# Kernel tuning notes

Hardware: AMD Instinct MI355X
Metric: run time of the kernel (lower is better)

## Reference

```python
import jax, jax.numpy as jnp
import numpy as np

N, E, F_IN, F_E, H, T = 100000, 1600000, 128, 16, 64, 32
NEG_SLOPE = 0.2


def setup_inputs() -> dict:
    key = jax.random.key(0)
    ks = jax.random.split(key, 24)
    s = 0.1
    inp = {
        'x': jax.random.normal(ks[0], (N, F_IN), jnp.float32),
        'edge_index': jax.random.randint(ks[1], (2, E), 0, N, dtype=jnp.int32),
        'edge_attr': jax.random.normal(ks[2], (E, F_E), jnp.float32),
        # GATConv layer 1 (heads=1)
        'W1': jax.random.normal(ks[3], (F_IN, H), jnp.float32) * s,
        'as1': jax.random.normal(ks[4], (H,), jnp.float32) * s,
        'ad1': jax.random.normal(ks[5], (H,), jnp.float32) * s,
        'We1': jax.random.normal(ks[6], (F_E, H), jnp.float32) * s,
        'ae1': jax.random.normal(ks[7], (H,), jnp.float32) * s,
        'b1': jnp.zeros((H,), jnp.float32),
        # GATConv layer 2
        'W2': jax.random.normal(ks[8], (H, H), jnp.float32) * s,
        'as2': jax.random.normal(ks[9], (H,), jnp.float32) * s,
        'ad2': jax.random.normal(ks[10], (H,), jnp.float32) * s,
        'We2': jax.random.normal(ks[11], (F_E, H), jnp.float32) * s,
        'ae2': jax.random.normal(ks[12], (H,), jnp.float32) * s,
        'b2': jnp.zeros((H,), jnp.float32),
        # classifier MLP (dropout in eval mode -> identity)
        'Wc1': jax.random.normal(ks[13], (H, H // 2), jnp.float32) * s,
        'bc1': jnp.zeros((H // 2,), jnp.float32),
        'Wc2': jax.random.normal(ks[14], (H // 2, T), jnp.float32) * s,
        'bc2': jnp.zeros((T,), jnp.float32),
    }
    return inp


def gat_conv(x, src, dst, edge_attr, W, a_s, a_d, We, a_e, b):
    """Single-head PyG-style GATConv with edge features and self-loops
    (self-loop edge_attr = mean of incoming edge_attr, fill_value='mean')."""
    n = x.shape[0]
    # self loops with mean incoming edge features
    deg = jax.ops.segment_sum(jnp.ones_like(dst, jnp.float32), dst, n)
    loop_attr = jax.ops.segment_sum(edge_attr, dst, n) / jnp.maximum(deg, 1.0)[:, None]
    loops = jnp.arange(n, dtype=src.dtype)
    src_f = jnp.concatenate([src, loops])
    dst_f = jnp.concatenate([dst, loops])
    ea = jnp.concatenate([edge_attr, loop_attr], axis=0)  # [E+N, F_E]
    h = x @ W                                             # [N, H]
    # attention logits per edge: alpha_src[j] + alpha_dst[i] + alpha_edge
    alpha = (h @ a_s)[src_f] + (h @ a_d)[dst_f] + (ea @ We) @ a_e
    alpha = jax.nn.leaky_relu(alpha, NEG_SLOPE)
    # segment softmax over incoming edges per destination node
    m = jax.ops.segment_max(alpha, dst_f, n)
    p = jnp.exp(alpha - m[dst_f])
    z = jax.ops.segment_sum(p, dst_f, n)
    w = p / z[dst_f]                                      # [E+N]
    out = jax.ops.segment_sum(w[:, None] * h[src_f], dst_f, n)
    return out + b


def reference(x, edge_index, edge_attr, W1, as1, ad1, We1, ae1, b1,
              W2, as2, ad2, We2, ae2, b2, Wc1, bc1, Wc2, bc2):
    src, dst = edge_index[0], edge_index[1]
    h = jax.nn.relu(gat_conv(x, src, dst, edge_attr, W1, as1, ad1, We1, ae1, b1))
    h = jax.nn.relu(gat_conv(h, src, dst, edge_attr, W2, as2, ad2, We2, ae2, b2))
    h = jax.nn.relu(h @ Wc1 + bc1)
    logits = h @ Wc2 + bc2
    return logits
```

## Files before the change

### kernel.cpp

```cpp
#include <hip/hip_runtime.h>
#include <hip/hip_bf16.h>
#include <hip/hip_fp16.h>

#define NEG_SLOPE 0.2f

__device__ __forceinline__ float leaky(float a) { return a > 0.f ? a : NEG_SLOPE * a; }

__global__ void compute_wvec(const float* __restrict__ We1, const float* __restrict__ ae1,
                             const float* __restrict__ We2, const float* __restrict__ ae2,
                             float* __restrict__ wv) {
    int t = threadIdx.x;
    if (t < 16) {
        float s = 0.f;
        for (int k = 0; k < 64; ++k) s += We1[t * 64 + k] * ae1[k];
        wv[t] = s;
    } else if (t < 32) {
        int f = t - 16;
        float s = 0.f;
        for (int k = 0; k < 64; ++k) s += We2[f * 64 + k] * ae2[k];
        wv[16 + f] = s;
    }
}

__global__ void pack_edges(const int* __restrict__ dst, const float* __restrict__ eattr,
                           const float* __restrict__ wv, int* __restrict__ deg,
                           uint2* __restrict__ meta, int E) {
    __shared__ float w1s[16], w2s[16];
    if (threadIdx.x < 16) w1s[threadIdx.x] = wv[threadIdx.x];
    else if (threadIdx.x < 32) w2s[threadIdx.x - 16] = wv[threadIdx.x];
    __syncthreads();
    int e = blockIdx.x * blockDim.x + threadIdx.x;
    if (e >= E) return;
    const float4* ep = (const float4*)(eattr + (size_t)e * 16);
    float4 q0 = ep[0], q1 = ep[1], q2 = ep[2], q3 = ep[3];
    float a[16] = {q0.x, q0.y, q0.z, q0.w, q1.x, q1.y, q1.z, q1.w,
                   q2.x, q2.y, q2.z, q2.w, q3.x, q3.y, q3.z, q3.w};
    float s1 = 0.f, s2 = 0.f;
#pragma unroll
    for (int f = 0; f < 16; ++f) { s1 += a[f] * w1s[f]; s2 += a[f] * w2s[f]; }
    unsigned int p1 = (unsigned int)__half_as_ushort(__float2half_rn(s1));
    unsigned int p2 = (unsigned int)__half_as_ushort(__float2half_rn(s2));
    int rank = atomicAdd(&deg[dst[e]], 1);
    meta[e] = make_uint2(p1 | (p2 << 16), (unsigned int)rank);
}

__global__ void scan_blocks(const int* __restrict__ deg, int* __restrict__ rowptr,
                            int* __restrict__ bsum, int n) {
    __shared__ int sh[1024];
    int i = blockIdx.x * 1024 + threadIdx.x;
    sh[threadIdx.x] = (i < n) ? deg[i] : 0;
    __syncthreads();
    for (int off = 1; off < 1024; off <<= 1) {
        int t = (threadIdx.x >= off) ? sh[threadIdx.x - off] : 0;
        __syncthreads();
        sh[threadIdx.x] += t;
        __syncthreads();
    }
    if (i < n) rowptr[i + 1] = sh[threadIdx.x];
    if (threadIdx.x == 1023) bsum[blockIdx.x] = sh[1023];
}

__global__ void scan_sums(int* __restrict__ bsum, int nb) {
    __shared__ int sh[1024];
    int t = threadIdx.x;
    int v = (t < nb) ? bsum[t] : 0;
    sh[t] = v;
    __syncthreads();
    for (int off = 1; off < 1024; off <<= 1) {
        int u = (t >= off) ? sh[t - off] : 0;
        __syncthreads();
        sh[t] += u;
        __syncthreads();
    }
    if (t < nb) bsum[t] = sh[t] - v;
}

__global__ void scan_finalize(int* __restrict__ rowptr, const int* __restrict__ bsum, int n) {
    int i = blockIdx.x * blockDim.x + threadIdx.x;
    if (i < n) rowptr[i + 1] += bsum[i >> 10];
    if (i == 0) rowptr[0] = 0;
}

__global__ __launch_bounds__(256) void route_edges(
    const int* __restrict__ src, const int* __restrict__ dst,
    const uint2* __restrict__ meta, const int* __restrict__ rowptr,
    uint2* __restrict__ recs, int E, int slice_sz) {
    int xcd = blockIdx.x & 7;
    int team = blockIdx.x >> 3;
    int teams = gridDim.x >> 3;
    int lo = xcd * slice_sz, hi = lo + slice_sz;
    for (int e = team * 256 + threadIdx.x; e < E; e += teams * 256) {
        int d = dst[e];
        if (d < lo || d >= hi) continue;
        uint2 m = meta[e];
        int pos = rowptr[d] + (int)m.y;
        recs[pos] = make_uint2((unsigned int)src[e], m.x);
    }
}

template <int K>
__global__ __launch_bounds__(256) void gemm_node(const float* __restrict__ X,
                                                 const float* __restrict__ W,
                                                 const float* __restrict__ a_s,
                                                 const float* __restrict__ a_d,
                                                 __half* __restrict__ Hout16,
                                                 float* __restrict__ ash,
                                                 float* __restrict__ adh, int n) {
    constexpr int KC = 64;
    __shared__ float xs[128 * 65];
    __shared__ float ws[KC * 64];
    int tid = threadIdx.x;
    int base = blockIdx.x * 128;
    int ct = tid & 7;
    int rt = tid >> 3;

    float acc[4][8];
#pragma unroll
    for (int i = 0; i < 4; ++i)
#pragma unroll
        for (int j = 0; j < 8; ++j) acc[i][j] = 0.f;

    for (int kc = 0; kc < K; kc += KC) {
#pragma unroll
        for (int p = 0; p < 8; ++p) {
            int idx = p * 256 + tid;
            int row = idx >> 4;
            int f4 = idx & 15;
            float4 q = make_float4(0.f, 0.f, 0.f, 0.f);
            if (base + row < n) q = *(const float4*)(X + (size_t)(base + row) * K + kc + f4 * 4);
            float* dp = xs + row * 65 + f4 * 4;
            dp[0] = q.x; dp[1] = q.y; dp[2] = q.z; dp[3] = q.w;
        }
#pragma unroll
        for (int p = 0; p < 4; ++p) {
            int idx = p * 256 + tid;
            int f = idx >> 4;
            int c4 = idx & 15;
            *(float4*)(ws + f * 64 + c4 * 4) =
                *(const float4*)(W + (size_t)(kc + f) * 64 + c4 * 4);
        }
        __syncthreads();
#pragma unroll 4
        for (int f = 0; f < KC; ++f) {
            float4 w0 = *(const float4*)(ws + f * 64 + ct * 8);
            float4 w1 = *(const float4*)(ws + f * 64 + ct * 8 + 4);
            float b0[8] = {w0.x, w0.y, w0.z, w0.w, w1.x, w1.y, w1.z, w1.w};
#pragma unroll
            for (int i = 0; i < 4; ++i) {
                float a = xs[(rt * 4 + i) * 65 + f];
#pragma unroll
                for (int j = 0; j < 8; ++j) acc[i][j] = fmaf(a, b0[j], acc[i][j]);
            }
        }
        __syncthreads();
    }

    float as_r[8], ad_r[8];
#pragma unroll
    for (int j = 0; j < 8; ++j) { as_r[j] = a_s[ct * 8 + j]; ad_r[j] = a_d[ct * 8 + j]; }
#pragma unroll
    for (int i = 0; i < 4; ++i) {
        int r = base + rt * 4 + i;
        float ps = 0.f, pd = 0.f;
#pragma unroll
        for (int j = 0; j < 8; ++j) {
            ps = fmaf(acc[i][j], as_r[j], ps);
            pd = fmaf(acc[i][j], ad_r[j], pd);
        }
        ps += __shfl_xor(ps, 1); pd += __shfl_xor(pd, 1);
        ps += __shfl_xor(ps, 2); pd += __shfl_xor(pd, 2);
        ps += __shfl_xor(ps, 4); pd += __shfl_xor(pd, 4);
        if (r < n) {
            union { __half h[8]; uint4 u; } pk;
#pragma unroll
            for (int j = 0; j < 8; ++j) pk.h[j] = __float2half_rn(acc[i][j]);
            *(uint4*)(Hout16 + (size_t)r * 64 + ct * 8) = pk.u;
            if (ct == 0) { ash[r] = ps; adh[r] = pd; }
        }
    }
}

template <int LAYER>
__global__ __launch_bounds__(256) void gat_aggregate(
    const __half* __restrict__ Hf, const float* __restrict__ ash, const float* __restrict__ adh,
    const int* __restrict__ rowptr, const uint2* __restrict__ recs,
    const float* __restrict__ bias, float* __restrict__ outp, int n) {
    int wave = threadIdx.x >> 6;
    int lane = threadIdx.x & 63;
    int i = blockIdx.x * 4 + wave;
    if (i >= n) return;
    int start = rowptr[i], end = rowptr[i + 1];
    float adi = adh[i];

    float acc = 0.f;
    float zl = 0.f, seal = 0.f;

    for (int c = start; c < end; c += 64) {
        int cnt = min(64, end - c);
        int s_l = 0;
        float p_l = 0.f;
        if (lane < cnt) {
            uint2 r = recs[c + lane];
            s_l = (int)r.x;
            unsigned short u = (LAYER == 0) ? (unsigned short)(r.y & 0xffffu)
                                            : (unsigned short)(r.y >> 16);
            float e = __half2float(__ushort_as_half(u));
            float p = __expf(leaky(ash[s_l] + adi + e));
            p_l = p;
            zl += p;
            seal += e;
        }
        int k = 0;
        for (; k + 4 <= cnt; k += 4) {
            int s0 = __builtin_amdgcn_readlane(s_l, k);
            int s1 = __builtin_amdgcn_readlane(s_l, k + 1);
            int s2 = __builtin_amdgcn_readlane(s_l, k + 2);
            int s3 = __builtin_amdgcn_readlane(s_l, k + 3);
            float p0 = __uint_as_float(__builtin_amdgcn_readlane((int)__float_as_uint(p_l), k));
            float p1 = __uint_as_float(__builtin_amdgcn_readlane((int)__float_as_uint(p_l), k + 1));
            float p2 = __uint_as_float(__builtin_amdgcn_readlane((int)__float_as_uint(p_l), k + 2));
            float p3 = __uint_as_float(__builtin_amdgcn_readlane((int)__float_as_uint(p_l), k + 3));
            float v0 = __half2float(Hf[(size_t)s0 * 64 + lane]);
            float v1 = __half2float(Hf[(size_t)s1 * 64 + lane]);
            float v2 = __half2float(Hf[(size_t)s2 * 64 + lane]);
            float v3 = __half2float(Hf[(size_t)s3 * 64 + lane]);
            acc = fmaf(p0, v0, acc);
            acc = fmaf(p1, v1, acc);
            acc = fmaf(p2, v2, acc);
            acc = fmaf(p3, v3, acc);
        }
        for (; k < cnt; ++k) {
            int s0 = __builtin_amdgcn_readlane(s_l, k);
            float p0 = __uint_as_float(__builtin_amdgcn_readlane((int)__float_as_uint(p_l), k));
            float v0 = __half2float(Hf[(size_t)s0 * 64 + lane]);
            acc = fmaf(p0, v0, acc);
        }
    }

    float z = zl, sea = seal;
#pragma unroll
    for (int off = 1; off < 64; off <<= 1) {
        z += __shfl_xor(z, off);
        sea += __shfl_xor(sea, off);
    }

    int d = end - start;
    float loop_sc = sea / (float)max(d, 1);
    float aself = leaky(ash[i] + adi + loop_sc);
    float pself = __expf(aself);
    z += pself;
    acc = fmaf(pself, __half2float(Hf[(size_t)i * 64 + lane]), acc);
    float o = acc / z + bias[lane];
    outp[(size_t)i * 64 + lane] = fmaxf(o, 0.f);
}

__global__ __launch_bounds__(256) void mlp_kernel(const float* __restrict__ X,
                                                  const float* __restrict__ Wc1,
                                                  const float* __restrict__ bc1,
                                                  const float* __restrict__ Wc2,
                                                  const float* __restrict__ bc2,
                                                  float* __restrict__ outp, int n) {
    __shared__ float v[8 * 64];
    __shared__ float tb[8 * 32];
    int base = blockIdx.x * 8;
    for (int t = threadIdx.x; t < 512; t += 256) {
        int r = t >> 6;
        v[t] = (base + r < n) ? X[(size_t)base * 64 + t] : 0.f;
    }
    __syncthreads();
    int r = threadIdx.x >> 5, j = threadIdx.x & 31;
    float acc = bc1[j];
#pragma unroll
    for (int k = 0; k < 64; ++k) acc += v[r * 64 + k] * Wc1[k * 32 + j];
    acc = fmaxf(acc, 0.f);
    tb[r * 32 + j] = acc;
    __syncthreads();
    float lg = bc2[j];
#pragma unroll
    for (int k2 = 0; k2 < 32; ++k2) lg += tb[r * 32 + k2] * Wc2[k2 * 32 + j];
    int row = base + r;
    if (row < n) outp[(size_t)row * 32 + j] = lg;
}

extern "C" void kernel_launch(void* const* d_in, const int* in_sizes, int n_in,
                              void* d_out, int out_size, void* d_ws, size_t ws_size,
                              hipStream_t stream) {
    const float* x    = (const float*)d_in[0];
    const int*   ei   = (const int*)d_in[1];
    const float* eatt = (const float*)d_in[2];
    const float* W1   = (const float*)d_in[3];
    const float* as1  = (const float*)d_in[4];
    const float* ad1  = (const float*)d_in[5];
    const float* We1  = (const float*)d_in[6];
    const float* ae1  = (const float*)d_in[7];
    const float* b1   = (const float*)d_in[8];
    const float* W2   = (const float*)d_in[9];
    const float* as2  = (const float*)d_in[10];
    const float* ad2  = (const float*)d_in[11];
    const float* We2  = (const float*)d_in[12];
    const float* ae2  = (const float*)d_in[13];
    const float* b2   = (const float*)d_in[14];
    const float* Wc1  = (const float*)d_in[15];
    const float* bc1  = (const float*)d_in[16];
    const float* Wc2  = (const float*)d_in[17];
    const float* bc2  = (const float*)d_in[18];

    int n = in_sizes[0] / 128;
    int E = in_sizes[1] / 2;
    const int* src = ei;
    const int* dst = ei + E;

    char* w = (char*)d_ws;
    auto alloc = [&](size_t bytes) { void* p = (void*)w; w += (bytes + 255) & ~(size_t)255; return p; };
    int* rowptr  = (int*)alloc((size_t)(n + 1) * 4);
    int* deg     = (int*)alloc((size_t)n * 4);
    int nb = (n + 1023) / 1024;
    int* bsum    = (int*)alloc((size_t)nb * 4);
    uint2* recs  = (uint2*)alloc((size_t)E * 8);
    uint2* meta  = (uint2*)alloc((size_t)E * 8);
    float* wv    = (float*)alloc(32 * 4);
    __half* hbuf16 = (__half*)alloc((size_t)n * 64 * 2);
    float* obuf  = (float*)alloc((size_t)n * 64 * 4);
    float* ash   = (float*)alloc((size_t)n * 4);
    float* adh   = (float*)alloc((size_t)n * 4);

    int slice_sz = (n + 7) / 8;

    hipMemsetAsync(deg, 0, (size_t)n * 4, stream);
    compute_wvec<<<1, 64, 0, stream>>>(We1, ae1, We2, ae2, wv);
    pack_edges<<<(E + 255) / 256, 256, 0, stream>>>(dst, eatt, wv, deg, meta, E);
    scan_blocks<<<nb, 1024, 0, stream>>>(deg, rowptr, bsum, n);
    scan_sums<<<1, 1024, 0, stream>>>(bsum, nb);
    scan_finalize<<<(n + 255) / 256, 256, 0, stream>>>(rowptr, bsum, n);
    route_edges<<<1024, 256, 0, stream>>>(src, dst, meta, rowptr, recs, E, slice_sz);

    gemm_node<128><<<(n + 127) / 128, 256, 0, stream>>>(x, W1, as1, ad1, hbuf16, ash, adh, n);
    gat_aggregate<0><<<(n + 3) / 4, 256, 0, stream>>>(hbuf16, ash, adh, rowptr, recs, b1, obuf, n);
    gemm_node<64><<<(n + 127) / 128, 256, 0, stream>>>(obuf, W2, as2, ad2, hbuf16, ash, adh, n);
    gat_aggregate<1><<<(n + 3) / 4, 256, 0, stream>>>(hbuf16, ash, adh, rowptr, recs, b2, obuf, n);
    mlp_kernel<<<(n + 7) / 8, 256, 0, stream>>>(obuf, Wc1, bc1, Wc2, bc2, (float*)d_out, n);
}
```

Before: 527.3 us.

## Fuse edge packing with first node GEMM and merge scan-sum into finalize

Runs edge packing and the layer-1 node GEMM inside one kernel, with odd blocks doing GEMM tiles and even blocks packing edges, so the two independent stages overlap and the separate wvec launch disappears (every packing block now recomputes the edge weight vectors itself). It also drops the single-block scan_sums kernel: each finalize block sums the preceding block totals on its own. This removes launches and serial gaps, at the cost of a large shared-memory footprint for all blocks, which limits occupancy for the packing half, plus some redundant per-block work.

```diff
diff --git a/kernel.cpp b/kernel.cpp
--- a/kernel.cpp
+++ b/kernel.cpp
@@ -6,42 +6,124 @@
 
 __device__ __forceinline__ float leaky(float a) { return a > 0.f ? a : NEG_SLOPE * a; }
 
-__global__ void compute_wvec(const float* __restrict__ We1, const float* __restrict__ ae1,
-                             const float* __restrict__ We2, const float* __restrict__ ae2,
-                             float* __restrict__ wv) {
-    int t = threadIdx.x;
-    if (t < 16) {
-        float s = 0.f;
-        for (int k = 0; k < 64; ++k) s += We1[t * 64 + k] * ae1[k];
-        wv[t] = s;
-    } else if (t < 32) {
-        int f = t - 16;
-        float s = 0.f;
-        for (int k = 0; k < 64; ++k) s += We2[f * 64 + k] * ae2[k];
-        wv[16 + f] = s;
-    }
-}
-
-__global__ void pack_edges(const int* __restrict__ dst, const float* __restrict__ eattr,
-                           const float* __restrict__ wv, int* __restrict__ deg,
-                           uint2* __restrict__ meta, int E) {
-    __shared__ float w1s[16], w2s[16];
-    if (threadIdx.x < 16) w1s[threadIdx.x] = wv[threadIdx.x];
-    else if (threadIdx.x < 32) w2s[threadIdx.x - 16] = wv[threadIdx.x];
-    __syncthreads();
-    int e = blockIdx.x * blockDim.x + threadIdx.x;
-    if (e >= E) return;
-    const float4* ep = (const float4*)(eattr + (size_t)e * 16);
-    float4 q0 = ep[0], q1 = ep[1], q2 = ep[2], q3 = ep[3];
-    float a[16] = {q0.x, q0.y, q0.z, q0.w, q1.x, q1.y, q1.z, q1.w,
-                   q2.x, q2.y, q2.z, q2.w, q3.x, q3.y, q3.z, q3.w};
-    float s1 = 0.f, s2 = 0.f;
-#pragma unroll
-    for (int f = 0; f < 16; ++f) { s1 += a[f] * w1s[f]; s2 += a[f] * w2s[f]; }
-    unsigned int p1 = (unsigned int)__half_as_ushort(__float2half_rn(s1));
-    unsigned int p2 = (unsigned int)__half_as_ushort(__float2half_rn(s2));
-    int rank = atomicAdd(&deg[dst[e]], 1);
-    meta[e] = make_uint2(p1 | (p2 << 16), (unsigned int)rank);
+__global__ __launch_bounds__(256) void fused_pack_gemm1(
+    const int* __restrict__ dst, const float* __restrict__ eattr,
+    const float* __restrict__ We1, const float* __restrict__ ae1,
+    const float* __restrict__ We2, const float* __restrict__ ae2,
+    int* __restrict__ deg, uint2* __restrict__ meta, int E,
+    const float* __restrict__ X, const float* __restrict__ W1,
+    const float* __restrict__ a_s, const float* __restrict__ a_d,
+    __half* __restrict__ Hout16, float* __restrict__ ash, float* __restrict__ adh, int n) {
+    __shared__ __align__(16) float sh[128 * 65 + 64 * 64];
+
+    if (blockIdx.x & 1) {
+        constexpr int K = 128, KC = 64;
+        float* xs = sh;
+        float* ws = sh + 128 * 65;
+        int tid = threadIdx.x;
+        int ct = tid & 7;
+        int rt = tid >> 3;
+        int ntiles = (n + 127) >> 7;
+        int stride = gridDim.x >> 1;
+        for (int tile = blockIdx.x >> 1; tile < ntiles; tile += stride) {
+            int base = tile * 128;
+            float acc[4][8];
+#pragma unroll
+            for (int i = 0; i < 4; ++i)
+#pragma unroll
+                for (int j = 0; j < 8; ++j) acc[i][j] = 0.f;
+
+            for (int kc = 0; kc < K; kc += KC) {
+#pragma unroll
+                for (int p = 0; p < 8; ++p) {
+                    int idx = p * 256 + tid;
+                    int row = idx >> 4;
+                    int f4 = idx & 15;
+                    float4 q = make_float4(0.f, 0.f, 0.f, 0.f);
+                    if (base + row < n) q = *(const float4*)(X + (size_t)(base + row) * K + kc + f4 * 4);
+                    float* dp = xs + row * 65 + f4 * 4;
+                    dp[0] = q.x; dp[1] = q.y; dp[2] = q.z; dp[3] = q.w;
+                }
+#pragma unroll
+                for (int p = 0; p < 4; ++p) {
+                    int idx = p * 256 + tid;
+                    int f = idx >> 4;
+                    int c4 = idx & 15;
+                    *(float4*)(ws + f * 64 + c4 * 4) =
+                        *(const float4*)(W1 + (size_t)(kc + f) * 64 + c4 * 4);
+                }
+                __syncthreads();
+#pragma unroll 4
+                for (int f = 0; f < KC; ++f) {
+                    float4 w0 = *(const float4*)(ws + f * 64 + ct * 8);
+                    float4 w1v = *(const float4*)(ws + f * 64 + ct * 8 + 4);
+                    float b0[8] = {w0.x, w0.y, w0.z, w0.w, w1v.x, w1v.y, w1v.z, w1v.w};
+#pragma unroll
+                    for (int i = 0; i < 4; ++i) {
+                        float a = xs[(rt * 4 + i) * 65 + f];
+#pragma unroll
+                        for (int j = 0; j < 8; ++j) acc[i][j] = fmaf(a, b0[j], acc[i][j]);
+                    }
+                }
+                __syncthreads();
+            }
+
+            float as_r[8], ad_r[8];
+#pragma unroll
+            for (int j = 0; j < 8; ++j) { as_r[j] = a_s[ct * 8 + j]; ad_r[j] = a_d[ct * 8 + j]; }
+#pragma unroll
+            for (int i = 0; i < 4; ++i) {
+                int r = base + rt * 4 + i;
+                float ps = 0.f, pd = 0.f;
+#pragma unroll
+                for (int j = 0; j < 8; ++j) {
+                    ps = fmaf(acc[i][j], as_r[j], ps);
+                    pd = fmaf(acc[i][j], ad_r[j], pd);
+                }
+                ps += __shfl_xor(ps, 1); pd += __shfl_xor(pd, 1);
+                ps += __shfl_xor(ps, 2); pd += __shfl_xor(pd, 2);
+                ps += __shfl_xor(ps, 4); pd += __shfl_xor(pd, 4);
+                if (r < n) {
+                    union { __half h[8]; uint4 u; } pk;
+#pragma unroll
+                    for (int j = 0; j < 8; ++j) pk.h[j] = __float2half_rn(acc[i][j]);
+                    *(uint4*)(Hout16 + (size_t)r * 64 + ct * 8) = pk.u;
+                    if (ct == 0) { ash[r] = ps; adh[r] = pd; }
+                }
+            }
+            __syncthreads();
+        }
+    } else {
+        int t = threadIdx.x;
+        if (t < 16) {
+            float s = 0.f;
+            for (int k = 0; k < 64; ++k) s += We1[t * 64 + k] * ae1[k];
+            sh[t] = s;
+        } else if (t < 32) {
+            int f = t - 16;
+            float s = 0.f;
+            for (int k = 0; k < 64; ++k) s += We2[f * 64 + k] * ae2[k];
+            sh[16 + f] = s;
+        }
+        __syncthreads();
+        int nch = (E + 255) >> 8;
+        int stride = (gridDim.x + 1) >> 1;
+        for (int ch = blockIdx.x >> 1; ch < nch; ch += stride) {
+            int e = ch * 256 + threadIdx.x;
+            if (e >= E) continue;
+            const float4* ep = (const float4*)(eattr + (size_t)e * 16);
+            float4 q0 = ep[0], q1 = ep[1], q2 = ep[2], q3 = ep[3];
+            float a[16] = {q0.x, q0.y, q0.z, q0.w, q1.x, q1.y, q1.z, q1.w,
+                           q2.x, q2.y, q2.z, q2.w, q3.x, q3.y, q3.z, q3.w};
+            float s1 = 0.f, s2 = 0.f;
+#pragma unroll
+            for (int f = 0; f < 16; ++f) { s1 += a[f] * sh[f]; s2 += a[f] * sh[16 + f]; }
+            unsigned int p1 = (unsigned int)__half_as_ushort(__float2half_rn(s1));
+            unsigned int p2 = (unsigned int)__half_as_ushort(__float2half_rn(s2));
+            int rank = atomicAdd(&deg[dst[e]], 1);
+            meta[e] = make_uint2(p1 | (p2 << 16), (unsigned int)rank);
+        }
+    }
 }
 
 __global__ void scan_blocks(const int* __restrict__ deg, int* __restrict__ rowptr,
@@ -60,25 +142,22 @@
     if (threadIdx.x == 1023) bsum[blockIdx.x] = sh[1023];
 }
 
-__global__ void scan_sums(int* __restrict__ bsum, int nb) {
-    __shared__ int sh[1024];
-    int t = threadIdx.x;
-    int v = (t < nb) ? bsum[t] : 0;
-    sh[t] = v;
+__global__ __launch_bounds__(256) void scan_finalize(int* __restrict__ rowptr,
+                                                     const int* __restrict__ bsum, int n) {
+    int b = blockIdx.x;
+    int local = 0;
+    for (int k = threadIdx.x; k < b; k += 256) local += bsum[k];
+#pragma unroll
+    for (int off = 1; off < 64; off <<= 1) local += __shfl_xor(local, off);
+    __shared__ int ws4[4];
+    if ((threadIdx.x & 63) == 0) ws4[threadIdx.x >> 6] = local;
     __syncthreads();
-    for (int off = 1; off < 1024; off <<= 1) {
-        int u = (t >= off) ? sh[t - off] : 0;
-        __syncthreads();
-        sh[t] += u;
-        __syncthreads();
-    }
-    if (t < nb) bsum[t] = sh[t] - v;
-}
-
-__global__ void scan_finalize(int* __restrict__ rowptr, const int* __restrict__ bsum, int n) {
-    int i = blockIdx.x * blockDim.x + threadIdx.x;
-    if (i < n) rowptr[i + 1] += bsum[i >> 10];
-    if (i == 0) rowptr[0] = 0;
+    int total = ws4[0] + ws4[1] + ws4[2] + ws4[3];
+    for (int r = threadIdx.x; r < 1024; r += 256) {
+        int i = b * 1024 + r;
+        if (i < n) rowptr[i + 1] += total;
+    }
+    if (b == 0 && threadIdx.x == 0) rowptr[0] = 0;
 }
 
 __global__ __launch_bounds__(256) void route_edges(
@@ -318,7 +397,6 @@
     int* bsum    = (int*)alloc((size_t)nb * 4);
     uint2* recs  = (uint2*)alloc((size_t)E * 8);
     uint2* meta  = (uint2*)alloc((size_t)E * 8);
-    float* wv    = (float*)alloc(32 * 4);
     __half* hbuf16 = (__half*)alloc((size_t)n * 64 * 2);
     float* obuf  = (float*)alloc((size_t)n * 64 * 4);
     float* ash   = (float*)alloc((size_t)n * 4);
@@ -327,14 +405,12 @@
     int slice_sz = (n + 7) / 8;
 
     hipMemsetAsync(deg, 0, (size_t)n * 4, stream);
-    compute_wvec<<<1, 64, 0, stream>>>(We1, ae1, We2, ae2, wv);
-    pack_edges<<<(E + 255) / 256, 256, 0, stream>>>(dst, eatt, wv, deg, meta, E);
+    fused_pack_gemm1<<<2048, 256, 0, stream>>>(dst, eatt, We1, ae1, We2, ae2, deg, meta, E,
+                                               x, W1, as1, ad1, hbuf16, ash, adh, n);
     scan_blocks<<<nb, 1024, 0, stream>>>(deg, rowptr, bsum, n);
-    scan_sums<<<1, 1024, 0, stream>>>(bsum, nb);
-    scan_finalize<<<(n + 255) / 256, 256, 0, stream>>>(rowptr, bsum, n);
+    scan_finalize<<<nb, 256, 0, stream>>>(rowptr, bsum, n);
     route_edges<<<1024, 256, 0, stream>>>(src, dst, meta, rowptr, recs, E, slice_sz);
 
-    gemm_node<128><<<(n + 127) / 128, 256, 0, stream>>>(x, W1, as1, ad1, hbuf16, ash, adh, n);
     gat_aggregate<0><<<(n + 3) / 4, 256, 0, stream>>>(hbuf16, ash, adh, rowptr, recs, b1, obuf, n);
     gemm_node<64><<<(n + 127) / 128, 256, 0, stream>>>(obuf, W2, as2, ad2, hbuf16, ash, adh, n);
     gat_aggregate<1><<<(n + 3) / 4, 256, 0, stream>>>(hbuf16, ash, adh, rowptr, recs, b2, obuf, n);
```

Result: faster. 506.8 us (-3.9%).

## Build CSR via two-level bucket sort with shared-memory histograms

Applied to the files above, without the earlier changes.

Replaces per-edge global atomic degree counting, multi-pass scans and the XCD-sliced routing pass with a block-local bucket histogram, column scans, a bucketed scatter and a per-bucket CSR build in shared memory. It also fuses the edge-weight vector computation into the counting kernel. The aim is to remove global atomic contention and the repeated full-edge reads from routing. In exchange it makes an extra pass over bucketed records, reuses the output buffer as scratch, and packs the local destination into the upper 8 bits of src, which assumes fewer than 16M nodes and at most 512 buckets.

```diff
diff --git a/kernel.cpp b/kernel.cpp
--- a/kernel.cpp
+++ b/kernel.cpp
@@ -3,98 +3,134 @@
 #include <hip/hip_fp16.h>
 
 #define NEG_SLOPE 0.2f
+#define EPB 8192
+#define NBUK 512
 
 __device__ __forceinline__ float leaky(float a) { return a > 0.f ? a : NEG_SLOPE * a; }
 
-__global__ void compute_wvec(const float* __restrict__ We1, const float* __restrict__ ae1,
-                             const float* __restrict__ We2, const float* __restrict__ ae2,
-                             float* __restrict__ wv) {
+__global__ __launch_bounds__(256) void count_pack(
+    const int* __restrict__ dst, const float* __restrict__ eattr,
+    const float* __restrict__ We1, const float* __restrict__ ae1,
+    const float* __restrict__ We2, const float* __restrict__ ae2,
+    unsigned int* __restrict__ meta_pay, int* __restrict__ counts, int E) {
+    __shared__ float wvs[32];
+    __shared__ int hist[NBUK];
+    int tid = threadIdx.x, i = blockIdx.x;
+    if (tid < 32) {
+        const float* Wp = (tid < 16) ? We1 : We2;
+        const float* ap = (tid < 16) ? ae1 : ae2;
+        int f = tid & 15;
+        float s = 0.f;
+        for (int k = 0; k < 64; ++k) s += Wp[f * 64 + k] * ap[k];
+        wvs[tid] = s;
+    }
+    for (int t = tid; t < NBUK; t += 256) hist[t] = 0;
+    __syncthreads();
+    int e0 = i * EPB, e1 = min(E, e0 + EPB);
+    for (int e = e0 + tid; e < e1; e += 256) {
+        int d = dst[e];
+        atomicAdd(&hist[d >> 8], 1);
+        const float4* ep = (const float4*)(eattr + (size_t)e * 16);
+        float4 q0 = ep[0], q1 = ep[1], q2 = ep[2], q3 = ep[3];
+        float a[16] = {q0.x, q0.y, q0.z, q0.w, q1.x, q1.y, q1.z, q1.w,
+                       q2.x, q2.y, q2.z, q2.w, q3.x, q3.y, q3.z, q3.w};
+        float s1 = 0.f, s2 = 0.f;
+#pragma unroll
+        for (int f = 0; f < 16; ++f) { s1 += a[f] * wvs[f]; s2 += a[f] * wvs[16 + f]; }
+        unsigned int p1 = (unsigned int)__half_as_ushort(__float2half_rn(s1));
+        unsigned int p2 = (unsigned int)__half_as_ushort(__float2half_rn(s2));
+        meta_pay[e] = p1 | (p2 << 16);
+    }
+    __syncthreads();
+    for (int t = tid; t < NBUK; t += 256) counts[(size_t)i * NBUK + t] = hist[t];
+}
+
+__global__ __launch_bounds__(256) void scan_cols(const int* __restrict__ counts,
+                                                 int* __restrict__ offsets,
+                                                 int* __restrict__ btot, int nblk) {
+    __shared__ int sh[256];
+    int b = blockIdx.x, t = threadIdx.x;
+    int v = (t < nblk) ? counts[(size_t)t * NBUK + b] : 0;
+    sh[t] = v;
+    __syncthreads();
+    for (int off = 1; off < 256; off <<= 1) {
+        int u = (t >= off) ? sh[t - off] : 0;
+        __syncthreads();
+        sh[t] += u;
+        __syncthreads();
+    }
+    if (t < nblk) offsets[(size_t)t * NBUK + b] = sh[t] - v;
+    if (t == 255) btot[b] = sh[255];
+}
+
+__global__ void scan_buckets(const int* __restrict__ btot, int* __restrict__ bbase,
+                             int* __restrict__ rowptr, int E, int n) {
+    __shared__ int sh[NBUK];
     int t = threadIdx.x;
-    if (t < 16) {
-        float s = 0.f;
-        for (int k = 0; k < 64; ++k) s += We1[t * 64 + k] * ae1[k];
-        wv[t] = s;
-    } else if (t < 32) {
-        int f = t - 16;
-        float s = 0.f;
-        for (int k = 0; k < 64; ++k) s += We2[f * 64 + k] * ae2[k];
-        wv[16 + f] = s;
-    }
-}
-
-__global__ void pack_edges(const int* __restrict__ dst, const float* __restrict__ eattr,
-                           const float* __restrict__ wv, int* __restrict__ deg,
-                           uint2* __restrict__ meta, int E) {
-    __shared__ float w1s[16], w2s[16];
-    if (threadIdx.x < 16) w1s[threadIdx.x] = wv[threadIdx.x];
-    else if (threadIdx.x < 32) w2s[threadIdx.x - 16] = wv[threadIdx.x];
-    __syncthreads();
-    int e = blockIdx.x * blockDim.x + threadIdx.x;
-    if (e >= E) return;
-    const float4* ep = (const float4*)(eattr + (size_t)e * 16);
-    float4 q0 = ep[0], q1 = ep[1], q2 = ep[2], q3 = ep[3];
-    float a[16] = {q0.x, q0.y, q0.z, q0.w, q1.x, q1.y, q1.z, q1.w,
-                   q2.x, q2.y, q2.z, q2.w, q3.x, q3.y, q3.z, q3.w};
-    float s1 = 0.f, s2 = 0.f;
-#pragma unroll
-    for (int f = 0; f < 16; ++f) { s1 += a[f] * w1s[f]; s2 += a[f] * w2s[f]; }
-    unsigned int p1 = (unsigned int)__half_as_ushort(__float2half_rn(s1));
-    unsigned int p2 = (unsigned int)__half_as_ushort(__float2half_rn(s2));
-    int rank = atomicAdd(&deg[dst[e]], 1);
-    meta[e] = make_uint2(p1 | (p2 << 16), (unsigned int)rank);
-}
-
-__global__ void scan_blocks(const int* __restrict__ deg, int* __restrict__ rowptr,
-                            int* __restrict__ bsum, int n) {
-    __shared__ int sh[1024];
-    int i = blockIdx.x * 1024 + threadIdx.x;
-    sh[threadIdx.x] = (i < n) ? deg[i] : 0;
-    __syncthreads();
-    for (int off = 1; off < 1024; off <<= 1) {
-        int t = (threadIdx.x >= off) ? sh[threadIdx.x - off] : 0;
-        __syncthreads();
-        sh[threadIdx.x] += t;
-        __syncthreads();
-    }
-    if (i < n) rowptr[i + 1] = sh[threadIdx.x];
-    if (threadIdx.x == 1023) bsum[blockIdx.x] = sh[1023];
-}
-
-__global__ void scan_sums(int* __restrict__ bsum, int nb) {
-    __shared__ int sh[1024];
-    int t = threadIdx.x;
-    int v = (t < nb) ? bsum[t] : 0;
+    int v = btot[t];
     sh[t] = v;
     __syncthreads();
-    for (int off = 1; off < 1024; off <<= 1) {
+    for (int off = 1; off < NBUK; off <<= 1) {
         int u = (t >= off) ? sh[t - off] : 0;
         __syncthreads();
         sh[t] += u;
         __syncthreads();
     }
-    if (t < nb) bsum[t] = sh[t] - v;
-}
-
-__global__ void scan_finalize(int* __restrict__ rowptr, const int* __restrict__ bsum, int n) {
-    int i = blockIdx.x * blockDim.x + threadIdx.x;
-    if (i < n) rowptr[i + 1] += bsum[i >> 10];
-    if (i == 0) rowptr[0] = 0;
-}
-
-__global__ __launch_bounds__(256) void route_edges(
-    const int* __restrict__ src, const int* __restrict__ dst,
-    const uint2* __restrict__ meta, const int* __restrict__ rowptr,
-    uint2* __restrict__ recs, int E, int slice_sz) {
-    int xcd = blockIdx.x & 7;
-    int team = blockIdx.x >> 3;
-    int teams = gridDim.x >> 3;
-    int lo = xcd * slice_sz, hi = lo + slice_sz;
-    for (int e = team * 256 + threadIdx.x; e < E; e += teams * 256) {
+    bbase[t] = sh[t] - v;
+    if (t == 0) rowptr[n] = E;
+}
+
+__global__ __launch_bounds__(256) void scatter_buckets(
+    const int* __restrict__ dst, const int* __restrict__ src,
+    const unsigned int* __restrict__ meta_pay, const int* __restrict__ offsets,
+    const int* __restrict__ bbase, uint2* __restrict__ bucketed, int E) {
+    __shared__ int cur[NBUK];
+    int i = blockIdx.x, tid = threadIdx.x;
+    for (int t = tid; t < NBUK; t += 256) cur[t] = bbase[t] + offsets[(size_t)i * NBUK + t];
+    __syncthreads();
+    int e0 = i * EPB, e1 = min(E, e0 + EPB);
+    for (int e = e0 + tid; e < e1; e += 256) {
         int d = dst[e];
-        if (d < lo || d >= hi) continue;
-        uint2 m = meta[e];
-        int pos = rowptr[d] + (int)m.y;
-        recs[pos] = make_uint2((unsigned int)src[e], m.x);
+        int slot = atomicAdd(&cur[d >> 8], 1);
+        bucketed[slot] = make_uint2((unsigned int)src[e] | ((unsigned int)(d & 255) << 24),
+                                    meta_pay[e]);
+    }
+}
+
+__global__ __launch_bounds__(256) void csr_build(const uint2* __restrict__ bucketed,
+                                                 const int* __restrict__ bbase,
+                                                 const int* __restrict__ btot,
+                                                 int* __restrict__ rowptr,
+                                                 uint2* __restrict__ recs, int n) {
+    __shared__ int deg[256], sc[256], cur[256];
+    int b = blockIdx.x, tid = threadIdx.x;
+    int base = bbase[b], cnt = btot[b];
+    deg[tid] = 0;
+    __syncthreads();
+    for (int k = tid; k < cnt; k += 256) {
+        uint2 r = bucketed[base + k];
+        atomicAdd(&deg[r.x >> 24], 1);
+    }
+    __syncthreads();
+    int dv = deg[tid];
+    sc[tid] = dv;
+    __syncthreads();
+    for (int off = 1; off < 256; off <<= 1) {
+        int u = (tid >= off) ? sc[tid - off] : 0;
+        __syncthreads();
+        sc[tid] += u;
+        __syncthreads();
+    }
+    int excl = sc[tid] - dv;
+    int d = b * 256 + tid;
+    if (d < n) rowptr[d] = base + excl;
+    cur[tid] = base + excl;
+    __syncthreads();
+    for (int k = tid; k < cnt; k += 256) {
+        uint2 r = bucketed[base + k];
+        int dl = (int)(r.x >> 24);
+        int pos = atomicAdd(&cur[dl], 1);
+        recs[pos] = make_uint2(r.x & 0x00FFFFFFu, r.y);
     }
 }
 
@@ -309,30 +345,28 @@
     int E = in_sizes[1] / 2;
     const int* src = ei;
     const int* dst = ei + E;
+    int nblk = (E + EPB - 1) / EPB;
 
     char* w = (char*)d_ws;
     auto alloc = [&](size_t bytes) { void* p = (void*)w; w += (bytes + 255) & ~(size_t)255; return p; };
-    int* rowptr  = (int*)alloc((size_t)(n + 1) * 4);
-    int* deg     = (int*)alloc((size_t)n * 4);
-    int nb = (n + 1023) / 1024;
-    int* bsum    = (int*)alloc((size_t)nb * 4);
-    uint2* recs  = (uint2*)alloc((size_t)E * 8);
-    uint2* meta  = (uint2*)alloc((size_t)E * 8);
-    float* wv    = (float*)alloc(32 * 4);
+    int* rowptr   = (int*)alloc((size_t)(n + 1) * 4);
+    int* counts   = (int*)alloc((size_t)nblk * NBUK * 4);
+    int* offsets  = (int*)alloc((size_t)nblk * NBUK * 4);
+    int* btot     = (int*)alloc((size_t)NBUK * 4);
+    int* bbase    = (int*)alloc((size_t)NBUK * 4);
+    unsigned int* meta_pay = (unsigned int*)alloc((size_t)E * 4);
+    uint2* recs   = (uint2*)alloc((size_t)E * 8);
     __half* hbuf16 = (__half*)alloc((size_t)n * 64 * 2);
-    float* obuf  = (float*)alloc((size_t)n * 64 * 4);
-    float* ash   = (float*)alloc((size_t)n * 4);
-    float* adh   = (float*)alloc((size_t)n * 4);
-
-    int slice_sz = (n + 7) / 8;
-
-    hipMemsetAsync(deg, 0, (size_t)n * 4, stream);
-    compute_wvec<<<1, 64, 0, stream>>>(We1, ae1, We2, ae2, wv);
-    pack_edges<<<(E + 255) / 256, 256, 0, stream>>>(dst, eatt, wv, deg, meta, E);
-    scan_blocks<<<nb, 1024, 0, stream>>>(deg, rowptr, bsum, n);
-    scan_sums<<<1, 1024, 0, stream>>>(bsum, nb);
-    scan_finalize<<<(n + 255) / 256, 256, 0, stream>>>(rowptr, bsum, n);
-    route_edges<<<1024, 256, 0, stream>>>(src, dst, meta, rowptr, recs, E, slice_sz);
+    float* obuf   = (float*)alloc((size_t)n * 64 * 4);
+    float* ash    = (float*)alloc((size_t)n * 4);
+    float* adh    = (float*)alloc((size_t)n * 4);
+    uint2* bucketed = (uint2*)obuf;
+
+    count_pack<<<nblk, 256, 0, stream>>>(dst, eatt, We1, ae1, We2, ae2, meta_pay, counts, E);
+    scan_cols<<<NBUK, 256, 0, stream>>>(counts, offsets, btot, nblk);
+    scan_buckets<<<1, NBUK, 0, stream>>>(btot, bbase, rowptr, E, n);
+    scatter_buckets<<<nblk, 256, 0, stream>>>(dst, src, meta_pay, offsets, bbase, bucketed, E);
+    csr_build<<<NBUK, 256, 0, stream>>>(bucketed, bbase, btot, rowptr, recs, n);
 
     gemm_node<128><<<(n + 127) / 128, 256, 0, stream>>>(x, W1, as1, ad1, hbuf16, ash, adh, n);
     gat_aggregate<0><<<(n + 3) / 4, 256, 0, stream>>>(hbuf16, ash, adh, rowptr, recs, b1, obuf, n);
```

Result: faster. 496.8 us (-5.8%).
